# Optimization experiments

Measured on AMD Instinct MI355X. Metric: run time of the kernel, lower is better.

## Reference

```python
import jax, jax.numpy as jnp
import numpy as np

N_USER = 100000
N_REPO = 100000


def _graph_conv(h_src, src, dst, n_src, n_dst, W, b):
    # DGL GraphConv, norm='both': D_dst^{-1/2} A^T D_src^{-1/2} (h W) + b
    ones = jnp.ones(src.shape[0], dtype=h_src.dtype)
    deg_out = jax.ops.segment_sum(ones, src, num_segments=n_src)
    deg_in = jax.ops.segment_sum(ones, dst, num_segments=n_dst)
    norm_src = jnp.where(deg_out > 0, deg_out ** -0.5, 0.0)
    norm_dst = jnp.where(deg_in > 0, deg_in ** -0.5, 0.0)
    feat = (h_src * norm_src[:, None]) @ W          # [n_src, out]
    agg = jax.ops.segment_sum(feat[src], dst, num_segments=n_dst)  # gather-scatter
    return agg * norm_dst[:, None] + b


def _cos_scores(hu, hr, u, v):
    nu = hu / jnp.linalg.norm(hu, axis=-1, keepdims=True).clip(1e-12)
    nr = hr / jnp.linalg.norm(hr, axis=-1, keepdims=True).clip(1e-12)
    return jnp.sum(nu[u] * nr[v], axis=-1)  # u_dot_v on normalized feats


def setup_inputs() -> dict:
    key = jax.random.key(0)
    ks = jax.random.split(key, 20)
    d_in, d_ur, d_hid, d_out = 256, 128, 128, 64
    s = 0.02
    inp = {
        'user_feat': jax.random.normal(ks[0], (N_USER, d_in), jnp.float32),
        'repo_feat': jax.random.normal(ks[1], (N_REPO, d_in), jnp.float32),
        'e_src': jax.random.randint(ks[2], (1600000,), 0, N_USER, jnp.int32),
        'e_dst': jax.random.randint(ks[3], (1600000,), 0, N_REPO, jnp.int32),
        'pos_u': jax.random.randint(ks[4], (200000,), 0, N_USER, jnp.int32),
        'pos_v': jax.random.randint(ks[5], (200000,), 0, N_REPO, jnp.int32),
        'neg_u': jax.random.randint(ks[6], (200000,), 0, N_USER, jnp.int32),
        'neg_v': jax.random.randint(ks[7], (200000,), 0, N_REPO, jnp.int32),
        # Embedding linears
        'W_ue': jax.random.normal(ks[8], (d_in, d_ur), jnp.float32) * s,
        'b_ue': jnp.zeros((d_ur,), jnp.float32),
        'W_re': jax.random.normal(ks[9], (d_in, d_ur), jnp.float32) * s,
        'b_re': jnp.zeros((d_ur,), jnp.float32),
        # hidden HeteroGraphConv: etype 'watch' (user->repo), 'watched-by' (repo->user)
        'W_h_ur': jax.random.normal(ks[10], (d_ur, d_hid), jnp.float32) * s,
        'b_h_ur': jnp.zeros((d_hid,), jnp.float32),
        'W_h_ru': jax.random.normal(ks[11], (d_ur, d_hid), jnp.float32) * s,
        'b_h_ru': jnp.zeros((d_hid,), jnp.float32),
        # out HeteroGraphConv
        'W_o_ur': jax.random.normal(ks[12], (d_hid, d_out), jnp.float32) * s,
        'b_o_ur': jnp.zeros((d_out,), jnp.float32),
        'W_o_ru': jax.random.normal(ks[13], (d_hid, d_out), jnp.float32) * s,
        'b_o_ru': jnp.zeros((d_out,), jnp.float32),
    }
    return inp


def reference(user_feat, repo_feat, e_src, e_dst, pos_u, pos_v, neg_u, neg_v,
              W_ue, b_ue, W_re, b_re, W_h_ur, b_h_ur, W_h_ru, b_h_ru,
              W_o_ur, b_o_ur, W_o_ru, b_o_ru):
    # embeddings (dropout is identity in eval / p=0)
    h_user = user_feat @ W_ue + b_ue
    h_repo = repo_feat @ W_re + b_re
    # hidden layer: each dst type receives from exactly one relation (sum agg trivial)
    h_repo1 = _graph_conv(h_user, e_src, e_dst, N_USER, N_REPO, W_h_ur, b_h_ur)
    h_user1 = _graph_conv(h_repo, e_dst, e_src, N_REPO, N_USER, W_h_ru, b_h_ru)
    # out layer
    out_repo = _graph_conv(h_user1, e_src, e_dst, N_USER, N_REPO, W_o_ur, b_o_ur)
    out_user = _graph_conv(h_repo1, e_dst, e_src, N_REPO, N_USER, W_o_ru, b_o_ru)
    pos_score = _cos_scores(out_user, out_repo, pos_u, pos_v)
    neg_score = _cos_scores(out_user, out_repo, neg_u, neg_v)
    return (pos_score, neg_score)
```

## Files before the change

### kernel.cpp

```cpp
#include <hip/hip_runtime.h>
#include <cstddef>
#include <cstdint>

#define N_NODES 100000
typedef unsigned int uint;
typedef unsigned short u16;
typedef __attribute__((ext_vector_type(8))) short bf16x8;
typedef __attribute__((ext_vector_type(4))) float f32x4;

__device__ __forceinline__ float bflo(uint u) { return __uint_as_float(u << 16); }
__device__ __forceinline__ float bfhi(uint u) { return __uint_as_float(u & 0xffff0000u); }
__device__ __forceinline__ uint bf_rne(float f) {
    uint u = __float_as_uint(f);
    return (u + 0x7fffu + ((u >> 16) & 1u)) >> 16;
}
__device__ __forceinline__ uint bfpack(float a, float b) {
    return bf_rne(a) | (bf_rne(b) << 16);
}
__device__ __forceinline__ void add8(float* a, uint4 u) {
    a[0] += bflo(u.x); a[1] += bfhi(u.x);
    a[2] += bflo(u.y); a[3] += bfhi(u.y);
    a[4] += bflo(u.z); a[5] += bfhi(u.z);
    a[6] += bflo(u.w); a[7] += bfhi(u.w);
}
union U4BF8 { uint4 u; bf16x8 b; };

#define HBINS 25000
#define NSL 128
__global__ __launch_bounds__(256) void hist_kernel(
    const int* __restrict__ src, const int* __restrict__ dst, int E,
    uint* __restrict__ partialU, uint* __restrict__ partialR) {
    __shared__ uint h[HBINS];
    int b = blockIdx.x;
    const int* ids = (b < NSL) ? src : dst;
    uint* out = ((b < NSL) ? partialU : partialR);
    int slice = (b < NSL) ? b : b - NSL;
    for (int i = threadIdx.x; i < HBINS; i += 256) h[i] = 0;
    __syncthreads();
    int per = (E + NSL - 1) / NSL;
    int lo = slice * per, hi = min(E, lo + per);
    for (int i = lo + threadIdx.x; i < hi; i += 256) {
        int id = ids[i];
        atomicAdd(&h[id >> 2], 1u << ((id & 3) * 8));
    }
    __syncthreads();
    out += (size_t)slice * HBINS;
    for (int i = threadIdx.x; i < HBINS; i += 256) out[i] = h[i];
}

__global__ __launch_bounds__(256) void histreduce(
    uint* __restrict__ partialU, uint* __restrict__ partialR,
    int* __restrict__ degU, int* __restrict__ degR) {
    int idx = blockIdx.x * blockDim.x + threadIdx.x;
    if (idx >= 2 * HBINS) return;
    uint* p = (idx < HBINS) ? partialU : partialR;
    int* deg = (idx < HBINS) ? degU : degR;
    int w = (idx < HBINS) ? idx : idx - HBINS;
    uint r0 = 0, r1 = 0, r2 = 0, r3 = 0;
    for (int b = 0; b < NSL; ++b) {
        size_t k = (size_t)b * HBINS + w;
        uint v = p[k];
        p[k] = r0 | (r1 << 8) | (r2 << 16) | (r3 << 24);
        r0 += v & 255u; r1 += (v >> 8) & 255u; r2 += (v >> 16) & 255u; r3 += v >> 24;
    }
    *(int4*)(deg + 4 * w) = make_int4((int)r0, (int)r1, (int)r2, (int)r3);
}

#define CHUNK 4096
#define SNB ((N_NODES + CHUNK - 1) / CHUNK)

__global__ __launch_bounds__(256) void scanA(
    const int* __restrict__ degU, const int* __restrict__ degR,
    int* __restrict__ bsum, int n) {
    int b = blockIdx.x;
    int side = b / SNB, blk = b % SNB;
    const int* deg = side ? degR : degU;
    int base = blk * CHUNK;
    int tid = threadIdx.x;
    int s = 0;
    #pragma unroll
    for (int k = 0; k < 16; ++k) {
        int i = base + k * 256 + tid;
        if (i < n) s += deg[i];
    }
    #pragma unroll
    for (int o = 32; o; o >>= 1) s += __shfl_xor(s, o);
    __shared__ int ws[4];
    if ((tid & 63) == 0) ws[tid >> 6] = s;
    __syncthreads();
    if (tid == 0) bsum[b] = ws[0] + ws[1] + ws[2] + ws[3];
}

__global__ void scanB(const int* __restrict__ bsum, int* __restrict__ bpre) {
    if (threadIdx.x == 0) {
        int run = 0;
        for (int i = 0; i < 2 * SNB; ++i) {
            if (i == SNB) run = 0;
            bpre[i] = run;
            run += bsum[i];
        }
    }
}

__global__ __launch_bounds__(256) void scanC(
    const int* __restrict__ degU, int* __restrict__ offU, float* __restrict__ normU,
    const int* __restrict__ degR, int* __restrict__ offR, float* __restrict__ normR,
    const int* __restrict__ bpre, int n) {
    int b = blockIdx.x;
    int side = b / SNB, blk = b % SNB;
    const int* deg = side ? degR : degU;
    int* off = side ? offR : offU;
    float* nrm = side ? normR : normU;
    int base = blk * CHUNK;
    int tid = threadIdx.x;
    int p0 = base + tid * 16;
    int e[16];
    #pragma unroll
    for (int k = 0; k < 16; ++k) {
        int i = p0 + k;
        e[k] = (i < n) ? deg[i] : 0;
    }
    int loc = 0;
    #pragma unroll
    for (int k = 0; k < 16; ++k) loc += e[k];
    int lane = tid & 63, wv = tid >> 6;
    int x = loc;
    #pragma unroll
    for (int o = 1; o < 64; o <<= 1) {
        int y = __shfl_up(x, o);
        if (lane >= o) x += y;
    }
    __shared__ int wsum[4];
    if (lane == 63) wsum[wv] = x;
    __syncthreads();
    int wvOff = 0;
    for (int i = 0; i < wv; ++i) wvOff += wsum[i];
    int run = bpre[b] + wvOff + (x - loc);
    if (blk == 0 && tid == 0) off[0] = 0;
    #pragma unroll
    for (int k = 0; k < 16; ++k) {
        int i = p0 + k;
        if (i < n) {
            int v = e[k];
            nrm[i] = (v > 0) ? (1.0f / sqrtf((float)v)) : 0.f;
            run += v;
            off[i + 1] = run;
        }
    }
}

__global__ __launch_bounds__(256) void fill_det(
    const int* __restrict__ src, const int* __restrict__ dst, int E,
    const uint* __restrict__ prefS, const uint* __restrict__ prefD,
    const int* __restrict__ offS, const int* __restrict__ offD,
    int* __restrict__ colS, int* __restrict__ colD) {
    __shared__ uint cur[3125];
    int b = blockIdx.x;
    int side = b >> 10;
    int r = b & 1023;
    int x = r & 7;
    int slice = r >> 3;
    const int* ids = side ? dst : src;
    const int* oth = side ? src : dst;
    const uint* pref = (side ? prefD : prefS) + (size_t)slice * HBINS;
    const int* off = side ? offD : offS;
    int* col = side ? colD : colS;
    for (int i = threadIdx.x; i < 3125; i += 256) cur[i] = 0;
    __syncthreads();
    int per = (E + NSL - 1) / NSL;
    int lo = slice * per, hi = min(E, lo + per);
    int rlo = x * 12500;
    for (int i = lo + threadIdx.x; i < hi; i += 256) {
        int id = ids[i];
        unsigned local = (unsigned)(id - rlo);
        if (local < 12500u) {
            int sh = (id & 3) * 8;
            uint old = atomicAdd(&cur[local >> 2], 1u << sh);
            int lrank = (old >> sh) & 255;
            int pbase = (pref[id >> 2] >> sh) & 255;
            col[off[id] + pbase + lrank] = oth[i];
        }
    }
}

__global__ void pre1_kernel(const float* __restrict__ W_ue, const float* __restrict__ W_h_ur,
                            const float* __restrict__ W_re, const float* __restrict__ W_h_ru,
                            const float* __restrict__ b_ue, const float* __restrict__ b_re,
                            float* __restrict__ T1a, float* __restrict__ T1b,
                            float* __restrict__ v1, float* __restrict__ v2) {
    int idx = blockIdx.x * blockDim.x + threadIdx.x;
    if (idx < 32768) {
        int k = idx >> 7, j = idx & 127;
        float acc = 0.f;
        for (int m = 0; m < 128; ++m) acc += W_ue[k * 128 + m] * W_h_ur[m * 128 + j];
        T1a[idx] = acc;
    } else if (idx < 65536) {
        int t = idx - 32768;
        int k = t >> 7, j = t & 127;
        float acc = 0.f;
        for (int m = 0; m < 128; ++m) acc += W_re[k * 128 + m] * W_h_ru[m * 128 + j];
        T1b[t] = acc;
    } else if (idx < 65664) {
        int j = idx - 65536;
        float acc = 0.f;
        for (int m = 0; m < 128; ++m) acc += b_ue[m] * W_h_ur[m * 128 + j];
        v1[j] = acc;
    } else if (idx < 65792) {
        int j = idx - 65664;
        float acc = 0.f;
        for (int m = 0; m < 128; ++m) acc += b_re[m] * W_h_ru[m * 128 + j];
        v2[j] = acc;
    }
}

__global__ void pre2_kernel(const float* __restrict__ T1a, const float* __restrict__ T1b,
                            const float* __restrict__ v1, const float* __restrict__ v2,
                            const float* __restrict__ W_o_ur, const float* __restrict__ W_o_ru,
                            const float* __restrict__ b_h_ur, const float* __restrict__ b_h_ru,
                            u16* __restrict__ Wt1, u16* __restrict__ Wt2,
                            float* __restrict__ bbig1, float* __restrict__ bbig2,
                            float* __restrict__ bvC, float* __restrict__ bvD) {
    int idx = blockIdx.x * blockDim.x + threadIdx.x;
    if (idx < 16384) {
        int k = idx >> 6, n = idx & 63;
        float acc = 0.f;
        for (int j = 0; j < 128; ++j) acc += T1a[k * 128 + j] * W_o_ru[j * 64 + n];
        Wt1[n * 256 + k] = (u16)bf_rne(acc);
    } else if (idx < 32768) {
        int t = idx - 16384;
        int k = t >> 6, n = t & 63;
        float acc = 0.f;
        for (int j = 0; j < 128; ++j) acc += T1b[k * 128 + j] * W_o_ur[j * 64 + n];
        Wt2[n * 256 + k] = (u16)bf_rne(acc);
    } else if (idx < 33024) {
        int t = idx - 32768;
        int n = t & 63, which = t >> 6;
        float acc = 0.f;
        if (which == 0)      { for (int j = 0; j < 128; ++j) acc += v1[j] * W_o_ru[j * 64 + n]; bbig1[n] = acc; }
        else if (which == 1) { for (int j = 0; j < 128; ++j) acc += v2[j] * W_o_ur[j * 64 + n]; bbig2[n] = acc; }
        else if (which == 2) { for (int j = 0; j < 128; ++j) acc += b_h_ru[j] * W_o_ur[j * 64 + n]; bvC[n] = acc; }
        else                 { for (int j = 0; j < 128; ++j) acc += b_h_ur[j] * W_o_ru[j * 64 + n]; bvD[n] = acc; }
    }
}

__global__ __launch_bounds__(256) void gemm_direct(
    const float* __restrict__ A1, const u16* __restrict__ Wt1,
    const float* __restrict__ bias1, const float* __restrict__ scale1,
    u16* __restrict__ out1,
    const float* __restrict__ A2, const u16* __restrict__ Wt2,
    const float* __restrict__ bias2, const float* __restrict__ scale2,
    u16* __restrict__ out2, int M, int half) {
    const float* A; const u16* Wt; const float* bias; const float* scale; u16* out;
    int blk = blockIdx.x;
    if (blk < half) { A = A1; Wt = Wt1; bias = bias1; scale = scale1; out = out1; }
    else { blk -= half; A = A2; Wt = Wt2; bias = bias2; scale = scale2; out = out2; }
    int tid = threadIdx.x;
    int w = tid >> 6, lane = tid & 63;
    int l15 = lane & 15, kch = lane >> 4;
    int grow = min(blk * 64 + w * 16 + l15, M - 1);
    const float* ar = A + (size_t)grow * 256;
    f32x4 acc[4];
    #pragma unroll
    for (int cf = 0; cf < 4; ++cf) acc[cf] = (f32x4){0.f, 0.f, 0.f, 0.f};
    #pragma unroll
    for (int ks = 0; ks < 8; ++ks) {
        int k0 = ks * 32 + kch * 8;
        float4 f0 = *(const float4*)(ar + k0);
        float4 f1 = *(const float4*)(ar + k0 + 4);
        U4BF8 a;
        a.u.x = bfpack(f0.x, f0.y); a.u.y = bfpack(f0.z, f0.w);
        a.u.z = bfpack(f1.x, f1.y); a.u.w = bfpack(f1.z, f1.w);
        #pragma unroll
        for (int cf = 0; cf < 4; ++cf) {
            const bf16x8 b = *(const bf16x8*)(Wt + (cf * 16 + l15) * 256 + k0);
            acc[cf] = __builtin_amdgcn_mfma_f32_16x16x32_bf16(a.b, b, acc[cf], 0, 0, 0);
        }
    }
    float bv[4];
    #pragma unroll
    for (int cf = 0; cf < 4; ++cf) bv[cf] = bias[cf * 16 + l15];
    #pragma unroll
    for (int r = 0; r < 4; ++r) {
        int orow = blk * 64 + w * 16 + kch * 4 + r;
        if (orow < M) {
            float n = scale[orow];
            #pragma unroll
            for (int cf = 0; cf < 4; ++cf) {
                float val = n * acc[cf][r] + n * bv[cf];
                out[(size_t)orow * 64 + cf * 16 + l15] = (u16)bf_rne(val);
            }
        }
    }
}

template <int MODE>
__global__ __launch_bounds__(256) void gather2(
    const uint* __restrict__ fA, const int* __restrict__ offA, const int* __restrict__ colA,
    const float* __restrict__ nmA, const float* __restrict__ bsA, uint* __restrict__ obA,
    const uint* __restrict__ fB, const int* __restrict__ offB, const int* __restrict__ colB,
    const float* __restrict__ nmB, const float* __restrict__ bsB, uint* __restrict__ obB,
    int n) {
    int node = (int)((blockIdx.x * (size_t)blockDim.x + threadIdx.x) >> 6);
    int lane = threadIdx.x & 63;
    if (node >= 2 * n) return;
    const uint* feat; const int* off; const int* col; const float* nmp; const float* bs;
    uint* ob;
    if (node < n) { feat = fA; off = offA; col = colA; nmp = nmA; bs = bsA; ob = obA; }
    else { node -= n; feat = fB; off = offB; col = colB; nmp = nmB; bs = bsB; ob = obB; }
    int g = lane >> 3, j = lane & 7;
    int b = off[node];
    int d = off[node + 1] - b;
    float acc[8] = {0.f, 0.f, 0.f, 0.f, 0.f, 0.f, 0.f, 0.f};
    for (int j0 = 0; j0 < d; j0 += 64) {
        int c = (j0 + lane < d) ? __builtin_nontemporal_load(col + b + j0 + lane) : 0;
        int cnt = min(64, d - j0);
        int k = 0;
        for (; k + 16 <= cnt; k += 16) {
            int s0 = __shfl(c, k + g);
            int s1 = __shfl(c, k + g + 8);
            uint4 u0 = *(const uint4*)(feat + (size_t)s0 * 32 + j * 4);
            uint4 u1 = *(const uint4*)(feat + (size_t)s1 * 32 + j * 4);
            add8(acc, u0); add8(acc, u1);
        }
        if (k + 8 <= cnt) {
            int s0 = __shfl(c, k + g);
            uint4 u0 = *(const uint4*)(feat + (size_t)s0 * 32 + j * 4);
            add8(acc, u0);
            k += 8;
        }
        if (k < cnt) {
            int rem = cnt - k;
            int sl = k + ((g < rem) ? g : 0);
            int s0 = __shfl(c, sl);
            if (g < rem) {
                uint4 u0 = *(const uint4*)(feat + (size_t)s0 * 32 + j * 4);
                add8(acc, u0);
            }
        }
    }
    #pragma unroll
    for (int o = 8; o < 64; o <<= 1)
        #pragma unroll
        for (int t = 0; t < 8; ++t) acc[t] += __shfl_xor(acc[t], o);
    float nm = nmp[node];
    float v[8];
    if (MODE == 0) {
        #pragma unroll
        for (int t = 0; t < 8; ++t) v[t] = nm * nm * acc[t] + nm * bs[8 * j + t];
    } else {
        float ss = 0.f;
        #pragma unroll
        for (int t = 0; t < 8; ++t) { v[t] = nm * acc[t] + bs[8 * j + t]; ss += v[t] * v[t]; }
        #pragma unroll
        for (int o = 1; o < 8; o <<= 1) ss += __shfl_xor(ss, o);
        float inv = 1.0f / fmaxf(sqrtf(ss), 1e-12f);
        #pragma unroll
        for (int t = 0; t < 8; ++t) v[t] *= inv;
    }
    if (g == 0) {
        uint4 o4;
        o4.x = bfpack(v[0], v[1]); o4.y = bfpack(v[2], v[3]);
        o4.z = bfpack(v[4], v[5]); o4.w = bfpack(v[6], v[7]);
        *(uint4*)(ob + (size_t)node * 32 + j * 4) = o4;
    }
}

__global__ __launch_bounds__(256) void score2(
    const uint* __restrict__ U, const uint* __restrict__ R,
    const int* __restrict__ pu, const int* __restrict__ pv,
    const int* __restrict__ nu, const int* __restrict__ nv,
    float* __restrict__ out, int P) {
    int wave = (int)((blockIdx.x * (size_t)blockDim.x + threadIdx.x) >> 6);
    int lane = threadIdx.x & 63;
    int half = lane >> 5, j = lane & 31;
    int pairIdx = wave * 2 + half;
    if (pairIdx >= 2 * P) return;
    int idx = (pairIdx < P) ? pairIdx : pairIdx - P;
    int u = (pairIdx < P) ? pu[idx] : nu[idx];
    int v = (pairIdx < P) ? pv[idx] : nv[idx];
    uint uu = U[(size_t)u * 32 + j];
    uint rr = R[(size_t)v * 32 + j];
    float p = bflo(uu) * bflo(rr) + bfhi(uu) * bfhi(rr);
#pragma unroll
    for (int o = 1; o < 32; o <<= 1) p += __shfl_xor(p, o);
    if (j == 0) out[pairIdx] = p;
}

extern "C" void kernel_launch(void* const* d_in, const int* in_sizes, int n_in,
                              void* d_out, int out_size, void* d_ws, size_t ws_size,
                              hipStream_t stream) {
    const float* user_feat = (const float*)d_in[0];
    const float* repo_feat = (const float*)d_in[1];
    const int*   e_src     = (const int*)d_in[2];
    const int*   e_dst     = (const int*)d_in[3];
    const int*   pos_u     = (const int*)d_in[4];
    const int*   pos_v     = (const int*)d_in[5];
    const int*   neg_u     = (const int*)d_in[6];
    const int*   neg_v     = (const int*)d_in[7];
    const float* W_ue      = (const float*)d_in[8];
    const float* b_ue      = (const float*)d_in[9];
    const float* W_re      = (const float*)d_in[10];
    const float* b_re      = (const float*)d_in[11];
    const float* W_h_ur    = (const float*)d_in[12];
    const float* b_h_ur    = (const float*)d_in[13];
    const float* W_h_ru    = (const float*)d_in[14];
    const float* b_h_ru    = (const float*)d_in[15];
    const float* W_o_ur    = (const float*)d_in[16];
    const float* b_o_ur    = (const float*)d_in[17];
    const float* W_o_ru    = (const float*)d_in[18];
    const float* b_o_ru    = (const float*)d_in[19];

    const int E  = in_sizes[2];
    const int P  = in_sizes[4];
    const int NN = N_NODES;

    char* wp = (char*)d_ws;
    auto alloc = [&](size_t bytes) -> char* {
        char* r = wp;
        wp += (bytes + 255) & ~(size_t)255;
        return r;
    };
    int* degU  = (int*)alloc(2 * (size_t)NN * sizeof(int));
    int* degR  = degU + NN;
    int* offU  = (int*)alloc((NN + 1) * sizeof(int));
    int* offR  = (int*)alloc((NN + 1) * sizeof(int));
    int* colS  = (int*)alloc((size_t)E * sizeof(int));
    int* colD  = (int*)alloc((size_t)E * sizeof(int));
    float* normU = (float*)alloc(2 * (size_t)NN * sizeof(float));
    float* normR = normU + NN;
    int* bsum  = (int*)alloc(2 * SNB * sizeof(int));
    int* bpre  = (int*)alloc(2 * SNB * sizeof(int));
    float* T1a   = (float*)alloc(32768 * sizeof(float));
    float* T1b   = (float*)alloc(32768 * sizeof(float));
    float* v1    = (float*)alloc(128 * sizeof(float));
    float* v2    = (float*)alloc(128 * sizeof(float));
    float* bbig1 = (float*)alloc(64 * sizeof(float));
    float* bbig2 = (float*)alloc(64 * sizeof(float));
    float* bvC   = (float*)alloc(64 * sizeof(float));
    float* bvD   = (float*)alloc(64 * sizeof(float));
    u16* Wt1     = (u16*)alloc(16384 * sizeof(u16));
    u16* Wt2     = (u16*)alloc(16384 * sizeof(u16));
    uint* bufA   = (uint*)alloc((size_t)NN * 32 * sizeof(uint));
    uint* bufB   = (uint*)alloc((size_t)NN * 32 * sizeof(uint));
    uint* bufC   = (uint*)alloc((size_t)NN * 32 * sizeof(uint));
    uint* bufD   = (uint*)alloc((size_t)NN * 32 * sizeof(uint));
    uint* partialU = bufA;
    uint* partialR = bufB;

    hist_kernel<<<2 * NSL, 256, 0, stream>>>(e_src, e_dst, E, partialU, partialR);
    histreduce<<<(2 * HBINS + 255) / 256, 256, 0, stream>>>(partialU, partialR, degU, degR);
    scanA<<<2 * SNB, 256, 0, stream>>>(degU, degR, bsum, NN);
    scanB<<<1, 64, 0, stream>>>(bsum, bpre);
    scanC<<<2 * SNB, 256, 0, stream>>>(degU, offU, normU, degR, offR, normR, bpre, NN);
    fill_det<<<2 * NSL * 8, 256, 0, stream>>>(e_src, e_dst, E, partialU, partialR,
                                              offU, offR, colS, colD);

    pre1_kernel<<<(65792 + 255) / 256, 256, 0, stream>>>(W_ue, W_h_ur, W_re, W_h_ru,
                                                         b_ue, b_re, T1a, T1b, v1, v2);
    pre2_kernel<<<(33024 + 255) / 256, 256, 0, stream>>>(T1a, T1b, v1, v2, W_o_ur, W_o_ru,
                                                         b_h_ur, b_h_ru, Wt1, Wt2,
                                                         bbig1, bbig2, bvC, bvD);

    const int half = (NN + 63) / 64;
    gemm_direct<<<2 * half, 256, 0, stream>>>(user_feat, Wt1, bbig1, normU, (u16*)bufA,
                                              repo_feat, Wt2, bbig2, normR, (u16*)bufB, NN, half);

    const int g2Grid = (int)(((size_t)2 * NN * 64 + 255) / 256);
    gather2<0><<<g2Grid, 256, 0, stream>>>(
        bufA, offR, colD, normR, bvD, bufC,
        bufB, offU, colS, normU, bvC, bufD, NN);

    gather2<1><<<g2Grid, 256, 0, stream>>>(
        bufC, offU, colS, normU, b_o_ru, bufA,
        bufD, offR, colD, normR, b_o_ur, bufB, NN);

    float* out = (float*)d_out;
    const int sGrid = (int)(((size_t)P * 64 + 255) / 256);
    score2<<<sGrid, 256, 0, stream>>>(bufA, bufB, pos_u, pos_v, neg_u, neg_v, out, P);
}
```

Baseline: 446.1 us.

## Switch intermediate features to fp16 with packed half2 accumulation in gathers

Intermediate node features are now stored as fp16 instead of bf16, and the gather kernels accumulate with packed half2 adds instead of unpacking to eight fp32 accumulators. This halves the ALU work per gathered row and cuts register use in the bandwidth-bound aggregation. The GEMM is also restructured to convert all A fragments first, then loop over output columns. Accumulating in fp16 risks precision loss and overflow on high-degree nodes.

```diff
diff --git a/kernel.cpp b/kernel.cpp
--- a/kernel.cpp
+++ b/kernel.cpp
@@ -1,4 +1,5 @@
 #include <hip/hip_runtime.h>
+#include <hip/hip_fp16.h>
 #include <cstddef>
 #include <cstdint>
 
@@ -17,13 +18,9 @@
 __device__ __forceinline__ uint bfpack(float a, float b) {
     return bf_rne(a) | (bf_rne(b) << 16);
 }
-__device__ __forceinline__ void add8(float* a, uint4 u) {
-    a[0] += bflo(u.x); a[1] += bfhi(u.x);
-    a[2] += bflo(u.y); a[3] += bfhi(u.y);
-    a[4] += bflo(u.z); a[5] += bfhi(u.z);
-    a[6] += bflo(u.w); a[7] += bfhi(u.w);
-}
 union U4BF8 { uint4 u; bf16x8 b; };
+union U4H   { uint4 u; __half2 h[4]; };
+union UH    { uint u; __half2 h; };
 
 #define HBINS 25000
 #define NSL 128
@@ -246,11 +243,11 @@
 __global__ __launch_bounds__(256) void gemm_direct(
     const float* __restrict__ A1, const u16* __restrict__ Wt1,
     const float* __restrict__ bias1, const float* __restrict__ scale1,
-    u16* __restrict__ out1,
+    uint* __restrict__ out1,
     const float* __restrict__ A2, const u16* __restrict__ Wt2,
     const float* __restrict__ bias2, const float* __restrict__ scale2,
-    u16* __restrict__ out2, int M, int half) {
-    const float* A; const u16* Wt; const float* bias; const float* scale; u16* out;
+    uint* __restrict__ out2, int M, int half) {
+    const float* A; const u16* Wt; const float* bias; const float* scale; uint* out;
     int blk = blockIdx.x;
     if (blk < half) { A = A1; Wt = Wt1; bias = bias1; scale = scale1; out = out1; }
     else { blk -= half; A = A2; Wt = Wt2; bias = bias2; scale = scale2; out = out2; }
@@ -259,21 +256,25 @@
     int l15 = lane & 15, kch = lane >> 4;
     int grow = min(blk * 64 + w * 16 + l15, M - 1);
     const float* ar = A + (size_t)grow * 256;
-    f32x4 acc[4];
-    #pragma unroll
-    for (int cf = 0; cf < 4; ++cf) acc[cf] = (f32x4){0.f, 0.f, 0.f, 0.f};
+    U4BF8 a[8];
     #pragma unroll
     for (int ks = 0; ks < 8; ++ks) {
         int k0 = ks * 32 + kch * 8;
         float4 f0 = *(const float4*)(ar + k0);
         float4 f1 = *(const float4*)(ar + k0 + 4);
-        U4BF8 a;
-        a.u.x = bfpack(f0.x, f0.y); a.u.y = bfpack(f0.z, f0.w);
-        a.u.z = bfpack(f1.x, f1.y); a.u.w = bfpack(f1.z, f1.w);
+        a[ks].u.x = bfpack(f0.x, f0.y); a[ks].u.y = bfpack(f0.z, f0.w);
+        a[ks].u.z = bfpack(f1.x, f1.y); a[ks].u.w = bfpack(f1.z, f1.w);
+    }
+    f32x4 acc[4];
+    #pragma unroll
+    for (int cf = 0; cf < 4; ++cf) acc[cf] = (f32x4){0.f, 0.f, 0.f, 0.f};
+    #pragma unroll
+    for (int cf = 0; cf < 4; ++cf) {
+        const u16* wrow = Wt + (cf * 16 + l15) * 256 + kch * 8;
         #pragma unroll
-        for (int cf = 0; cf < 4; ++cf) {
-            const bf16x8 b = *(const bf16x8*)(Wt + (cf * 16 + l15) * 256 + k0);
-            acc[cf] = __builtin_amdgcn_mfma_f32_16x16x32_bf16(a.b, b, acc[cf], 0, 0, 0);
+        for (int ks = 0; ks < 8; ++ks) {
+            const bf16x8 b = *(const bf16x8*)(wrow + ks * 32);
+            acc[cf] = __builtin_amdgcn_mfma_f32_16x16x32_bf16(a[ks].b, b, acc[cf], 0, 0, 0);
         }
     }
     float bv[4];
@@ -287,7 +288,8 @@
             #pragma unroll
             for (int cf = 0; cf < 4; ++cf) {
                 float val = n * acc[cf][r] + n * bv[cf];
-                out[(size_t)orow * 64 + cf * 16 + l15] = (u16)bf_rne(val);
+                UH hh; hh.h = __floats2half2_rn(val, 0.f);
+                ((u16*)out)[(size_t)orow * 64 + cf * 16 + l15] = (u16)(hh.u & 0xffffu);
             }
         }
     }
@@ -310,7 +312,8 @@
     int g = lane >> 3, j = lane & 7;
     int b = off[node];
     int d = off[node + 1] - b;
-    float acc[8] = {0.f, 0.f, 0.f, 0.f, 0.f, 0.f, 0.f, 0.f};
+    __half2 hz = __floats2half2_rn(0.f, 0.f);
+    __half2 hacc[4] = {hz, hz, hz, hz};
     for (int j0 = 0; j0 < d; j0 += 64) {
         int c = (j0 + lane < d) ? __builtin_nontemporal_load(col + b + j0 + lane) : 0;
         int cnt = min(64, d - j0);
@@ -318,14 +321,19 @@
         for (; k + 16 <= cnt; k += 16) {
             int s0 = __shfl(c, k + g);
             int s1 = __shfl(c, k + g + 8);
-            uint4 u0 = *(const uint4*)(feat + (size_t)s0 * 32 + j * 4);
-            uint4 u1 = *(const uint4*)(feat + (size_t)s1 * 32 + j * 4);
-            add8(acc, u0); add8(acc, u1);
+            U4H u0, u1;
+            u0.u = *(const uint4*)(feat + (size_t)s0 * 32 + j * 4);
+            u1.u = *(const uint4*)(feat + (size_t)s1 * 32 + j * 4);
+            #pragma unroll
+            for (int t = 0; t < 4; ++t) hacc[t] = __hadd2(hacc[t], u0.h[t]);
+            #pragma unroll
+            for (int t = 0; t < 4; ++t) hacc[t] = __hadd2(hacc[t], u1.h[t]);
         }
         if (k + 8 <= cnt) {
             int s0 = __shfl(c, k + g);
-            uint4 u0 = *(const uint4*)(feat + (size_t)s0 * 32 + j * 4);
-            add8(acc, u0);
+            U4H u0; u0.u = *(const uint4*)(feat + (size_t)s0 * 32 + j * 4);
+            #pragma unroll
+            for (int t = 0; t < 4; ++t) hacc[t] = __hadd2(hacc[t], u0.h[t]);
             k += 8;
         }
         if (k < cnt) {
@@ -333,24 +341,35 @@
             int sl = k + ((g < rem) ? g : 0);
             int s0 = __shfl(c, sl);
             if (g < rem) {
-                uint4 u0 = *(const uint4*)(feat + (size_t)s0 * 32 + j * 4);
-                add8(acc, u0);
+                U4H u0; u0.u = *(const uint4*)(feat + (size_t)s0 * 32 + j * 4);
+                #pragma unroll
+                for (int t = 0; t < 4; ++t) hacc[t] = __hadd2(hacc[t], u0.h[t]);
             }
         }
     }
     #pragma unroll
-    for (int o = 8; o < 64; o <<= 1)
+    for (int o = 8; o < 64; o <<= 1) {
         #pragma unroll
-        for (int t = 0; t < 8; ++t) acc[t] += __shfl_xor(acc[t], o);
+        for (int t = 0; t < 4; ++t) {
+            UH x; x.h = hacc[t];
+            x.u = (uint)__shfl_xor((int)x.u, o);
+            hacc[t] = __hadd2(hacc[t], x.h);
+        }
+    }
     float nm = nmp[node];
     float v[8];
+    #pragma unroll
+    for (int t = 0; t < 4; ++t) {
+        float2 f = __half22float2(hacc[t]);
+        v[2 * t] = f.x; v[2 * t + 1] = f.y;
+    }
     if (MODE == 0) {
         #pragma unroll
-        for (int t = 0; t < 8; ++t) v[t] = nm * nm * acc[t] + nm * bs[8 * j + t];
+        for (int t = 0; t < 8; ++t) v[t] = nm * nm * v[t] + nm * bs[8 * j + t];
     } else {
         float ss = 0.f;
         #pragma unroll
-        for (int t = 0; t < 8; ++t) { v[t] = nm * acc[t] + bs[8 * j + t]; ss += v[t] * v[t]; }
+        for (int t = 0; t < 8; ++t) { v[t] = nm * v[t] + bs[8 * j + t]; ss += v[t] * v[t]; }
         #pragma unroll
         for (int o = 1; o < 8; o <<= 1) ss += __shfl_xor(ss, o);
         float inv = 1.0f / fmaxf(sqrtf(ss), 1e-12f);
@@ -358,10 +377,12 @@
         for (int t = 0; t < 8; ++t) v[t] *= inv;
     }
     if (g == 0) {
-        uint4 o4;
-        o4.x = bfpack(v[0], v[1]); o4.y = bfpack(v[2], v[3]);
-        o4.z = bfpack(v[4], v[5]); o4.w = bfpack(v[6], v[7]);
-        *(uint4*)(ob + (size_t)node * 32 + j * 4) = o4;
+        U4H o4;
+        o4.h[0] = __floats2half2_rn(v[0], v[1]);
+        o4.h[1] = __floats2half2_rn(v[2], v[3]);
+        o4.h[2] = __floats2half2_rn(v[4], v[5]);
+        o4.h[3] = __floats2half2_rn(v[6], v[7]);
+        *(uint4*)(ob + (size_t)node * 32 + j * 4) = o4.u;
     }
 }
 
@@ -378,9 +399,12 @@
     int idx = (pairIdx < P) ? pairIdx : pairIdx - P;
     int u = (pairIdx < P) ? pu[idx] : nu[idx];
     int v = (pairIdx < P) ? pv[idx] : nv[idx];
-    uint uu = U[(size_t)u * 32 + j];
-    uint rr = R[(size_t)v * 32 + j];
-    float p = bflo(uu) * bflo(rr) + bfhi(uu) * bfhi(rr);
+    UH uu, rr;
+    uu.u = U[(size_t)u * 32 + j];
+    rr.u = R[(size_t)v * 32 + j];
+    float2 fu = __half22float2(uu.h);
+    float2 fr = __half22float2(rr.h);
+    float p = fu.x * fr.x + fu.y * fr.y;
 #pragma unroll
     for (int o = 1; o < 32; o <<= 1) p += __shfl_xor(p, o);
     if (j == 0) out[pairIdx] = p;
@@ -462,8 +486,8 @@
                                                          bbig1, bbig2, bvC, bvD);
 
     const int half = (NN + 63) / 64;
-    gemm_direct<<<2 * half, 256, 0, stream>>>(user_feat, Wt1, bbig1, normU, (u16*)bufA,
-                                              repo_feat, Wt2, bbig2, normR, (u16*)bufB, NN, half);
+    gemm_direct<<<2 * half, 256, 0, stream>>>(user_feat, Wt1, bbig1, normU, bufA,
+                                              repo_feat, Wt2, bbig2, normR, bufB, NN, half);
 
     const int g2Grid = (int)(((size_t)2 * NN * 64 + 255) / 256);
     gather2<0><<<g2Grid, 256, 0, stream>>>(
```

After: 428.4 us. 1.04x faster.
